# Optimization experiments

Measured on AMD Instinct MI355X. Metric: run time of the kernel, lower is better.

The kernel has to match this reference:

```python
import jax, jax.numpy as jnp
import numpy as np

EPS = 1e-8
ALPHA = 1.0


def setup_inputs() -> dict:
    key = jax.random.key(0)
    k1, k2 = jax.random.split(key)
    N = 8192
    pred = jax.random.normal(k1, (N,), dtype=jnp.float32)
    gt = jax.random.normal(k2, (N,), dtype=jnp.float32)
    return {"pred": pred, "gt": gt, "n": N}


def _rank_counts(x):
    # sa[i] = #{j : x[i] > x[j]}  (pairwise O(N^2) comparison, reduced per row)
    return jnp.sum((x[:, None] > x[None, :]).astype(x.dtype), axis=-1)


def reference(pred, gt, n):
    N = pred.shape[0]
    sa = _rank_counts(pred)                 # [N]
    sb = _rank_counts(gt)                   # [N]
    delta = (sa - sb) / (N + EPS)           # rank disagreement, normalized
    a2 = jax.lax.stop_gradient(pred) - delta * ALPHA  # pred.detach() - delta*alpha
    l = jnp.abs(pred - a2)                  # L1, reduction='none'
    return jnp.sum(l) / n
```

## Files before the change

### kernel.cpp

```cpp
#include <hip/hip_runtime.h>


constexpr int T    = 1024;
constexpr int NI   = 32;
constexpr int NN   = 8192;
constexpr int JW   = 64;
constexpr unsigned BIAS   = 0x40000000u;
constexpr unsigned POISON = 0xAAAAAAAAu;

__global__ __launch_bounds__(T) void score_loss_one(
    const float* __restrict__ pred,
    const float* __restrict__ gt,
    unsigned* __restrict__ bsum,
    float* __restrict__ out,
    double inv)
{
    __shared__ float sw[NN];
    __shared__ int dsum[NI];
    __shared__ unsigned wred[16];

    const int tid  = threadIdx.x;
    const int b    = blockIdx.x;
    const int il4  = tid & 7;
    const int s    = tid >> 3;
    const int ib   = b * NI + il4 * 4;

    float xi[4], yi[4];
#pragma unroll
    for (int c = 0; c < 4; ++c) { xi[c] = pred[ib + c]; yi[c] = gt[ib + c]; }

    if (tid < NI) dsum[tid] = 0;

    int d[4] = {0, 0, 0, 0};

    {
        const float4* src = reinterpret_cast<const float4*>(pred);
        float4* dst = reinterpret_cast<float4*>(sw);
#pragma unroll
        for (int k = 0; k < (NN / 4) / T; ++k)
            dst[k * T + tid] = src[k * T + tid];
    }
    __syncthreads();
    {
        const float4* w = reinterpret_cast<const float4*>(sw + s * JW);
#pragma unroll
        for (int t = 0; t < JW / 4; ++t) {
            float4 p = w[t];
#pragma unroll
            for (int c = 0; c < 4; ++c)
                d[c] += (xi[c] > p.x) + (xi[c] > p.y) + (xi[c] > p.z) + (xi[c] > p.w);
        }
    }
    __syncthreads();

    {
        const float4* src = reinterpret_cast<const float4*>(gt);
        float4* dst = reinterpret_cast<float4*>(sw);
#pragma unroll
        for (int k = 0; k < (NN / 4) / T; ++k)
            dst[k * T + tid] = src[k * T + tid];
    }
    __syncthreads();
    {
        const float4* w = reinterpret_cast<const float4*>(sw + s * JW);
#pragma unroll
        for (int t = 0; t < JW / 4; ++t) {
            float4 g = w[t];
#pragma unroll
            for (int c = 0; c < 4; ++c)
                d[c] -= (yi[c] > g.x) + (yi[c] > g.y) + (yi[c] > g.z) + (yi[c] > g.w);
        }
    }

#pragma unroll
    for (int c = 0; c < 4; ++c) {
#pragma unroll
        for (int off = 8; off < 64; off <<= 1)
            d[c] += __shfl_xor(d[c], off, 64);
    }
    if ((tid & 63) < 8) {
#pragma unroll
        for (int c = 0; c < 4; ++c)
            atomicAdd(&dsum[il4 * 4 + c], d[c]);
    }
    __syncthreads();

    if (tid < NI) {
        int v = dsum[tid];
        v = (v < 0) ? -v : v;
#pragma unroll
        for (int off = 16; off >= 1; off >>= 1)
            v += __shfl_xor(v, off, 64);
        if (tid == 0)
            __hip_atomic_store(&bsum[b], (unsigned)v + BIAS,
                               __ATOMIC_RELEASE, __HIP_MEMORY_SCOPE_AGENT);
    }

    if (b == 0) {
        __syncthreads();
        const int nb = gridDim.x;
        unsigned acc = 0;
        if (tid < nb) {
            unsigned v;
            for (;;) {
                v = __hip_atomic_load(&bsum[tid], __ATOMIC_ACQUIRE,
                                      __HIP_MEMORY_SCOPE_AGENT);
                if (v != 0u && v != POISON) break;
                __builtin_amdgcn_s_sleep(2);
            }
            acc = v - BIAS;
        }
        for (int off = 1; off < 64; off <<= 1)
            acc += __shfl_xor(acc, off, 64);
        if ((tid & 63) == 0) wred[tid >> 6] = acc;
        __syncthreads();
        if (tid == 0) {
            unsigned tot = 0;
#pragma unroll
            for (int w = 0; w < 16; ++w) tot += wred[w];
            out[0] = (float)((double)tot * inv);
        }
    }
}

extern "C" void kernel_launch(void* const* d_in, const int* in_sizes, int n_in,
                              void* d_out, int out_size, void* d_ws, size_t ws_size,
                              hipStream_t stream)
{
    const float* pred = (const float*)d_in[0];
    const float* gt   = (const float*)d_in[1];
    const int N = in_sizes[0];

    float* out     = (float*)d_out;
    unsigned* bsum = (unsigned*)d_ws;

    const double inv = 1.0 / (((double)N + 1e-8) * (double)N);

    dim3 grid(N / NI);
    score_loss_one<<<grid, T, 0, stream>>>(pred, gt, bsum, out, inv);
}
```

Baseline: 17.72 us.

## Replace brute-force rank counting with per-block bitonic sort and binary search

Each block now bitonic-sorts the 8192 values into 128 chunks of 64 in shared memory using wave shuffles, then counts ranks by binary search within each chunk instead of comparing each element against every value. This removes the O(N) compare loop per element but adds redundant sorting in every one of the 256 blocks, plus shuffle-heavy network work and divergent LDS searches. The grid-wide completion check now uses a biased range test instead of poison/zero values, with a shorter sleep.

```diff
diff --git a/kernel.cpp b/kernel.cpp
--- a/kernel.cpp
+++ b/kernel.cpp
@@ -1,93 +1,93 @@
 #include <hip/hip_runtime.h>
 
 
-constexpr int T    = 1024;
-constexpr int NI   = 32;
-constexpr int NN   = 8192;
-constexpr int JW   = 64;
-constexpr unsigned BIAS   = 0x40000000u;
-constexpr unsigned POISON = 0xAAAAAAAAu;
+constexpr int T   = 1024;
+constexpr int NN  = 8192;
+constexpr int NC  = 128;
+constexpr int CS  = 64;
+constexpr int NI  = 32;
+constexpr unsigned BIAS = 0x40000000u;
 
-__global__ __launch_bounds__(T) void score_loss_one(
+__global__ __launch_bounds__(T) void score_loss_sort(
     const float* __restrict__ pred,
     const float* __restrict__ gt,
     unsigned* __restrict__ bsum,
     float* __restrict__ out,
     double inv)
 {
-    __shared__ float sw[NN];
-    __shared__ int dsum[NI];
+    __shared__ float sv[NN + CS];
+    __shared__ int dsh[NI];
     __shared__ unsigned wred[16];
 
     const int tid  = threadIdx.x;
     const int b    = blockIdx.x;
-    const int il4  = tid & 7;
-    const int s    = tid >> 3;
-    const int ib   = b * NI + il4 * 4;
+    const int wave = tid >> 6;
+    const int lane = tid & 63;
+    const int il   = tid >> 5;
+    const int r    = tid & 31;
+    const int i    = b * NI + il;
 
-    float xi[4], yi[4];
+    const float xi = pred[i];
+    const float yi = gt[i];
+
+    auto sort_phase = [&](const float* __restrict__ src) {
+        float v[8];
+        const int c0 = wave * 8;
 #pragma unroll
-    for (int c = 0; c < 4; ++c) { xi[c] = pred[ib + c]; yi[c] = gt[ib + c]; }
+        for (int rp = 0; rp < 8; ++rp)
+            v[rp] = src[(c0 + rp) * CS + lane];
+#pragma unroll
+        for (int k = 2; k <= 64; k <<= 1) {
+#pragma unroll
+            for (int j = k >> 1; j > 0; j >>= 1) {
+                const bool keepmin = (((lane & j) == 0) == ((lane & k) == 0));
+#pragma unroll
+                for (int rp = 0; rp < 8; ++rp) {
+                    float o  = __shfl_xor(v[rp], j, 64);
+                    float mn = fminf(v[rp], o);
+                    float mx = fmaxf(v[rp], o);
+                    v[rp] = keepmin ? mn : mx;
+                }
+            }
+        }
+#pragma unroll
+        for (int rp = 0; rp < 8; ++rp)
+            sv[(c0 + rp) * CS + lane] = v[rp];
+    };
 
-    if (tid < NI) dsum[tid] = 0;
+    auto search4 = [&](float x) -> int {
+        int tot = 0;
+#pragma unroll
+        for (int q = 0; q < 4; ++q) {
+            const float* arr = sv + (r * 4 + q) * CS;
+            int lo = 0;
+#pragma unroll
+            for (int st = 64; st >= 1; st >>= 1) {
+                bool ok = (lo + st <= 64) && (arr[lo + st - 1] < x);
+                lo += ok ? st : 0;
+            }
+            tot += lo;
+        }
+        return tot;
+    };
 
-    int d[4] = {0, 0, 0, 0};
-
-    {
-        const float4* src = reinterpret_cast<const float4*>(pred);
-        float4* dst = reinterpret_cast<float4*>(sw);
-#pragma unroll
-        for (int k = 0; k < (NN / 4) / T; ++k)
-            dst[k * T + tid] = src[k * T + tid];
-    }
+    sort_phase(pred);
     __syncthreads();
-    {
-        const float4* w = reinterpret_cast<const float4*>(sw + s * JW);
-#pragma unroll
-        for (int t = 0; t < JW / 4; ++t) {
-            float4 p = w[t];
-#pragma unroll
-            for (int c = 0; c < 4; ++c)
-                d[c] += (xi[c] > p.x) + (xi[c] > p.y) + (xi[c] > p.z) + (xi[c] > p.w);
-        }
-    }
+    int d = search4(xi);
     __syncthreads();
 
-    {
-        const float4* src = reinterpret_cast<const float4*>(gt);
-        float4* dst = reinterpret_cast<float4*>(sw);
-#pragma unroll
-        for (int k = 0; k < (NN / 4) / T; ++k)
-            dst[k * T + tid] = src[k * T + tid];
-    }
+    sort_phase(gt);
     __syncthreads();
-    {
-        const float4* w = reinterpret_cast<const float4*>(sw + s * JW);
-#pragma unroll
-        for (int t = 0; t < JW / 4; ++t) {
-            float4 g = w[t];
-#pragma unroll
-            for (int c = 0; c < 4; ++c)
-                d[c] -= (yi[c] > g.x) + (yi[c] > g.y) + (yi[c] > g.z) + (yi[c] > g.w);
-        }
-    }
+    d -= search4(yi);
 
 #pragma unroll
-    for (int c = 0; c < 4; ++c) {
-#pragma unroll
-        for (int off = 8; off < 64; off <<= 1)
-            d[c] += __shfl_xor(d[c], off, 64);
-    }
-    if ((tid & 63) < 8) {
-#pragma unroll
-        for (int c = 0; c < 4; ++c)
-            atomicAdd(&dsum[il4 * 4 + c], d[c]);
-    }
+    for (int off = 1; off < 32; off <<= 1)
+        d += __shfl_xor(d, off, 64);
+    if (r == 0) dsh[il] = (d < 0) ? -d : d;
     __syncthreads();
 
     if (tid < NI) {
-        int v = dsum[tid];
-        v = (v < 0) ? -v : v;
+        int v = dsh[tid];
 #pragma unroll
         for (int off = 16; off >= 1; off >>= 1)
             v += __shfl_xor(v, off, 64);
@@ -98,17 +98,17 @@
 
     if (b == 0) {
         __syncthreads();
-        const int nb = gridDim.x;
         unsigned acc = 0;
-        if (tid < nb) {
-            unsigned v;
+        if (tid < 256) {
+            unsigned v, diff;
             for (;;) {
                 v = __hip_atomic_load(&bsum[tid], __ATOMIC_ACQUIRE,
                                       __HIP_MEMORY_SCOPE_AGENT);
-                if (v != 0u && v != POISON) break;
-                __builtin_amdgcn_s_sleep(2);
+                diff = v - BIAS;
+                if (diff <= 262144u) break;
+                __builtin_amdgcn_s_sleep(1);
             }
-            acc = v - BIAS;
+            acc = diff;
         }
         for (int off = 1; off < 64; off <<= 1)
             acc += __shfl_xor(acc, off, 64);
@@ -137,5 +137,5 @@
     const double inv = 1.0 / (((double)N + 1e-8) * (double)N);
 
     dim3 grid(N / NI);
-    score_loss_one<<<grid, T, 0, stream>>>(pred, gt, bsum, out, inv);
+    score_loss_sort<<<grid, T, 0, stream>>>(pred, gt, bsum, out, inv);
 }
```

Result: slower. 42.84 us (+141.8%).
